# Optimization experiments

Measured on AMD Instinct MI355X. Metric: run time of the kernel, lower is better.

The kernel has to match this reference:

```python
import jax, jax.numpy as jnp
import numpy as np

N_LAYERS = 3
LEAKY_ALPHA = 0.2
NEG_INF = -9e15

U, I, E_ENT, R = 50000, 25000, 80000, 20
D, K, N_EDGES, BATCH = 64, 16, 4000000, 16384


def setup_inputs() -> dict:
    key = jax.random.key(0)
    ks = jax.random.split(key, 16)
    return {
        "users": jax.random.randint(ks[0], (BATCH,), 0, U),
        "items": jax.random.randint(ks[1], (BATCH,), 0, I),
        "g_rows": jax.random.randint(ks[2], (N_EDGES,), 0, U + I, dtype=jnp.int32),
        "g_cols": jax.random.randint(ks[3], (N_EDGES,), 0, U + I, dtype=jnp.int32),
        "g_vals": jax.random.uniform(ks[4], (N_EDGES,), jnp.float32) * (1.0 / 27.0),
        "user_emb": jax.random.normal(ks[5], (U, D), jnp.float32) * 0.1,
        "item_emb": jax.random.normal(ks[6], (I, D), jnp.float32) * 0.1,
        "entity_emb": jax.random.normal(ks[7], (E_ENT + 1, D), jnp.float32) * 0.1,
        "relation_emb": jax.random.normal(ks[8], (R + 1, D), jnp.float32) * 0.1,
        "kg_entities": jax.random.randint(ks[9], (I, K), 0, E_ENT + 1, dtype=jnp.int32),
        "kg_relations": jax.random.randint(ks[10], (I, K), 0, R, dtype=jnp.int32),
        "fc_W": jax.random.normal(ks[11], (2 * D, D), jnp.float32) * (1.0 / np.sqrt(2 * D)),
        "fc_b": jnp.zeros((D,), jnp.float32),
    }


def _gat_item_embs(item_emb, entity_emb, relation_emb, kg_entities, kg_relations, fc_W, fc_b):
    # GAT.forward_relation over fixed-width padded KG neighbor sets
    ent = entity_emb[kg_entities]        # [I, K, D]
    rel = relation_emb[kg_relations]     # [I, K, D]
    Wh = jnp.broadcast_to(item_emb[:, None, :], ent.shape)
    a_input = jnp.concatenate([Wh, ent], axis=-1)           # [I, K, 2D]
    e = jnp.sum((a_input @ fc_W + fc_b) * rel, axis=-1)     # [I, K]
    e = jax.nn.leaky_relu(e, LEAKY_ALPHA)
    mask = kg_entities != (entity_emb.shape[0] - 1)         # padding id == num_entities
    e = jnp.where(mask, e, NEG_INF)
    att = jax.nn.softmax(e, axis=1)                         # softmax per item over neighbors
    return jnp.einsum('ik,ikd->id', att, ent) + item_emb    # residual


def _lightgcn(user_emb, items_kg, g_rows, g_cols, g_vals):
    all_emb = jnp.concatenate([user_emb, items_kg], axis=0)  # [N, D]
    n = all_emb.shape[0]
    acc = all_emb
    for _ in range(N_LAYERS):
        all_emb = jax.ops.segment_sum(g_vals[:, None] * all_emb[g_cols], g_rows, num_segments=n)
        acc = acc + all_emb
    return acc / (N_LAYERS + 1)  # mean over layer outputs


def reference(users, items, g_rows, g_cols, g_vals, user_emb, item_emb,
              entity_emb, relation_emb, kg_entities, kg_relations, fc_W, fc_b):
    items_kg = _gat_item_embs(item_emb, entity_emb, relation_emb,
                              kg_entities, kg_relations, fc_W, fc_b)
    light = _lightgcn(user_emb, items_kg, g_rows, g_cols, g_vals)
    num_users = user_emb.shape[0]
    u = light[users]
    it = light[num_users + items]
    return jnp.sum(u * it, axis=1)  # gamma [batch]
```

## Files before the change

kernel.cpp:

```cpp
#include <hip/hip_runtime.h>

#define D 64
#define NEG_INF -9e15f
#define MAXK 16
#define BSH 6
#define BROWS 64
#define MAXNB 2048
#define SCAP 4096
#define SBSH 4
#define MAXNSB 128
#define SBB 8

__device__ __forceinline__ unsigned short f2bf(float f) {
    unsigned u = __float_as_uint(f);
    return (unsigned short)((u + 0x7FFFu + ((u >> 16) & 1u)) >> 16);
}
__device__ __forceinline__ float bf2f(unsigned short h) {
    return __uint_as_float(((unsigned)h) << 16);
}

__global__ void relpre_kernel(const float* __restrict__ fc_W, const float* __restrict__ fc_b,
                              const float* __restrict__ rel_emb,
                              float* __restrict__ w1r, float* __restrict__ w2r,
                              float* __restrict__ br) {
    int r = blockIdx.x;
    int j = threadIdx.x;
    const float* rr = rel_emb + r * D;
    float s1 = 0.f, s2 = 0.f;
    for (int d = 0; d < D; ++d) {
        float rv = rr[d];
        s1 += fc_W[j * D + d] * rv;
        s2 += fc_W[(D + j) * D + d] * rv;
    }
    w1r[r * D + j] = s1;
    w2r[r * D + j] = s2;
    if (j == 0) {
        float sb = 0.f;
        for (int d = 0; d < D; ++d) sb += fc_b[d] * rr[d];
        br[r] = sb;
    }
}

__global__ void gat16_kernel(const float* __restrict__ item_emb, const float* __restrict__ ent_emb,
                             const int* __restrict__ kg_e, const int* __restrict__ kg_r,
                             const float* __restrict__ w1r, const float* __restrict__ w2r,
                             const float* __restrict__ br,
                             float* __restrict__ x_items, unsigned short* __restrict__ xb_items,
                             int I, int pad_id) {
    const int K = 16;
    int wave = (blockIdx.x * blockDim.x + threadIdx.x) >> 6;
    int lane = threadIdx.x & 63;
    if (wave >= I) return;
    int i = wave;
    float itemv = item_emb[i * D + lane];
    float entv[16], pp[16], brv[16];
    int eidx_[16];
    #pragma unroll
    for (int k = 0; k < K; ++k) {
        int eidx = kg_e[i * K + k];
        int r = kg_r[i * K + k];
        eidx_[k] = eidx;
        float ev = ent_emb[(long)eidx * D + lane];
        entv[k] = ev;
        pp[k] = itemv * w1r[r * D + lane] + ev * w2r[r * D + lane];
        brv[k] = br[r];
    }
    float e[16];
    #pragma unroll
    for (int k = 0; k < K; ++k) {
        float p = pp[k];
        #pragma unroll
        for (int off = 32; off > 0; off >>= 1) p += __shfl_xor(p, off, 64);
        p += brv[k];
        p = p > 0.f ? p : 0.2f * p;
        if (eidx_[k] == pad_id) p = NEG_INF;
        e[k] = p;
    }
    float m = e[0];
    #pragma unroll
    for (int k = 1; k < K; ++k) m = fmaxf(m, e[k]);
    float s = 0.f;
    float att[16];
    #pragma unroll
    for (int k = 0; k < K; ++k) { att[k] = expf(e[k] - m); s += att[k]; }
    float inv = 1.f / s;
    float o = itemv;
    #pragma unroll
    for (int k = 0; k < K; ++k) o += att[k] * inv * entv[k];
    x_items[(long)i * D + lane] = o;
    if (xb_items) xb_items[(long)i * D + lane] = f2bf(o);
}

__global__ void gat_kernel(const float* __restrict__ item_emb, const float* __restrict__ ent_emb,
                           const int* __restrict__ kg_e, const int* __restrict__ kg_r,
                           const float* __restrict__ w1r, const float* __restrict__ w2r,
                           const float* __restrict__ br,
                           float* __restrict__ x_items, unsigned short* __restrict__ xb_items,
                           int I, int K, int pad_id) {
    int wave = (blockIdx.x * blockDim.x + threadIdx.x) >> 6;
    int lane = threadIdx.x & 63;
    if (wave >= I) return;
    int i = wave;
    float itemv = item_emb[i * D + lane];
    float entv[MAXK];
    float e[MAXK];
    for (int k = 0; k < K; ++k) {
        int eidx = kg_e[i * K + k];
        int r = kg_r[i * K + k];
        float ev = ent_emb[(long)eidx * D + lane];
        entv[k] = ev;
        float p = itemv * w1r[r * D + lane] + ev * w2r[r * D + lane];
        #pragma unroll
        for (int off = 32; off > 0; off >>= 1) p += __shfl_xor(p, off, 64);
        p += br[r];
        p = p > 0.f ? p : 0.2f * p;
        if (eidx == pad_id) p = NEG_INF;
        e[k] = p;
    }
    float m = e[0];
    for (int k = 1; k < K; ++k) m = fmaxf(m, e[k]);
    float s = 0.f;
    float att[MAXK];
    for (int k = 0; k < K; ++k) { att[k] = expf(e[k] - m); s += att[k]; }
    float inv = 1.f / s;
    float o = itemv;
    for (int k = 0; k < K; ++k) o += att[k] * inv * entv[k];
    x_items[(long)i * D + lane] = o;
    if (xb_items) xb_items[(long)i * D + lane] = f2bf(o);
}

__global__ void initmark_kernel(const float* __restrict__ user_emb, float* __restrict__ x0,
                                unsigned short* __restrict__ xb,
                                const int* __restrict__ users, const int* __restrict__ items,
                                int* __restrict__ flags, int* __restrict__ rowlist,
                                int* __restrict__ nlist, int U, int B, int n4) {
    int i = blockIdx.x * blockDim.x + threadIdx.x;
    if (i < n4) {
        float4 v = ((const float4*)user_emb)[i];
        ((float4*)x0)[i] = v;
        if (xb) {
            ushort4 m;
            m.x = f2bf(v.x); m.y = f2bf(v.y); m.z = f2bf(v.z); m.w = f2bf(v.w);
            ((ushort4*)xb)[i] = m;
        }
    }
    if (i < B) {
        int r1 = users[i];
        if (atomicExch(&flags[r1], 1) == 0) rowlist[atomicAdd(nlist, 1)] = r1;
        int r2 = U + items[i];
        if (atomicExch(&flags[r2], 1) == 0) rowlist[atomicAdd(nlist, 1)] = r2;
    }
}

__global__ void init_kernel(const float* __restrict__ user_emb,
                            float* __restrict__ x, float* __restrict__ acc,
                            int UD, int ND) {
    for (int idx = blockIdx.x * blockDim.x + threadIdx.x; idx < ND;
         idx += gridDim.x * blockDim.x) {
        float v = (idx < UD) ? user_emb[idx] : x[idx];
        x[idx] = v;
        acc[idx] = v;
    }
}

__global__ void mark_kernel(const int* __restrict__ users, const int* __restrict__ items,
                            int* __restrict__ flags, int* __restrict__ rowlist,
                            int* __restrict__ nlist, int U, int B) {
    int i = blockIdx.x * blockDim.x + threadIdx.x;
    if (i >= B) return;
    int r1 = users[i];
    if (atomicExch(&flags[r1], 1) == 0) rowlist[atomicAdd(nlist, 1)] = r1;
    int r2 = U + items[i];
    if (atomicExch(&flags[r2], 1) == 0) rowlist[atomicAdd(nlist, 1)] = r2;
}

__global__ void bhist_kernel(const int* __restrict__ rows, int* __restrict__ bcnt,
                             int n_edges, int NB) {
    __shared__ int h[MAXNB];
    for (int i = threadIdx.x; i < NB; i += blockDim.x) h[i] = 0;
    __syncthreads();
    for (int e = blockIdx.x * blockDim.x + threadIdx.x; e < n_edges;
         e += gridDim.x * blockDim.x)
        atomicAdd(&h[rows[e] >> BSH], 1);
    __syncthreads();
    for (int i = threadIdx.x; i < NB; i += blockDim.x)
        if (h[i]) atomicAdd(&bcnt[i], h[i]);
}

__global__ void bscan_kernel(const int* __restrict__ bcnt, int* __restrict__ bstart,
                             int* __restrict__ bfill, int* __restrict__ sbfill,
                             int NB, int n_edges) {
    __shared__ int bufA[MAXNB];
    __shared__ int bufB[MAXNB];
    int tid = threadIdx.x;
    int v0 = (tid < NB) ? bcnt[tid] : 0;
    int v1 = (tid + 1024 < NB) ? bcnt[tid + 1024] : 0;
    bufA[tid] = v0;
    bufA[tid + 1024] = v1;
    __syncthreads();
    int* src = bufA;
    int* dst = bufB;
    for (int off = 1; off < MAXNB; off <<= 1) {
        int j0 = tid, j1 = tid + 1024;
        dst[j0] = src[j0] + (j0 >= off ? src[j0 - off] : 0);
        dst[j1] = src[j1] + (j1 >= off ? src[j1 - off] : 0);
        __syncthreads();
        int* t = src; src = dst; dst = t;
    }
    if (tid < NB) {
        int ex = src[tid] - v0;
        bstart[tid] = ex;
        bfill[tid] = ex;
        if ((tid & ((1 << SBSH) - 1)) == 0) sbfill[tid >> SBSH] = ex;
    }
    if (tid + 1024 < NB) {
        int ex = src[tid + 1024] - v1;
        bstart[tid + 1024] = ex;
        bfill[tid + 1024] = ex;
        if (((tid + 1024) & ((1 << SBSH) - 1)) == 0) sbfill[(tid + 1024) >> SBSH] = ex;
    }
    if (tid == 0) bstart[NB] = n_edges;
}

__global__ __launch_bounds__(1024) void
part1_kernel(const int* __restrict__ rows, const int* __restrict__ cols,
             const float* __restrict__ vals,
             int* __restrict__ sbfill, long* __restrict__ etmp,
             int n_edges, int NSB) {
    __shared__ int h[MAXNSB];
    int nb_blocks = gridDim.x;
    int c0 = (int)((long)n_edges * blockIdx.x / nb_blocks);
    int c1 = (int)((long)n_edges * (blockIdx.x + 1) / nb_blocks);
    for (int i = threadIdx.x; i < NSB; i += blockDim.x) h[i] = 0;
    __syncthreads();
    for (int e = c0 + threadIdx.x; e < c1; e += blockDim.x)
        atomicAdd(&h[rows[e] >> (BSH + SBSH)], 1);
    __syncthreads();
    for (int i = threadIdx.x; i < NSB; i += blockDim.x)
        if (h[i]) h[i] = atomicAdd(&sbfill[i], h[i]);
    __syncthreads();
    for (int e = c0 + threadIdx.x; e < c1; e += blockDim.x) {
        int r = rows[e];
        int pos = atomicAdd(&h[r >> (BSH + SBSH)], 1);
        etmp[pos] = ((long)(unsigned)__float_as_int(vals[e]) << 32)
                  | (unsigned)(cols[e] | ((r & (BROWS - 1)) << 20)
                               | (((r >> BSH) & ((1 << SBSH) - 1)) << 26));
    }
}

__global__ __launch_bounds__(256) void
part2_kernel(const long* __restrict__ etmp, const int* __restrict__ bstart,
             int* __restrict__ bfill, long* __restrict__ edges2, int NB) {
    __shared__ int h[1 << SBSH];
    int sb = blockIdx.x / SBB;
    int j  = blockIdx.x % SBB;
    int b0 = sb << SBSH;
    int b1 = b0 + (1 << SBSH); if (b1 > NB) b1 = NB;
    int s = bstart[b0];
    int t = bstart[b1];
    int m = t - s;
    int c0 = s + (int)((long)m * j / SBB);
    int c1 = s + (int)((long)m * (j + 1) / SBB);
    if (threadIdx.x < (1 << SBSH)) h[threadIdx.x] = 0;
    __syncthreads();
    for (int e = c0 + threadIdx.x; e < c1; e += blockDim.x)
        atomicAdd(&h[((int)etmp[e] >> 26) & ((1 << SBSH) - 1)], 1);
    __syncthreads();
    if (threadIdx.x < (1 << SBSH)) {
        int c = h[threadIdx.x];
        if (c) h[threadIdx.x] = atomicAdd(&bfill[b0 + threadIdx.x], c);
    }
    __syncthreads();
    for (int e = c0 + threadIdx.x; e < c1; e += blockDim.x) {
        long v = etmp[e];
        int pos = atomicAdd(&h[((int)v >> 26) & ((1 << SBSH) - 1)], 1);
        edges2[pos] = v;
    }
}

__global__ __launch_bounds__(256) void
part_legacy_kernel(const int* __restrict__ rows, const int* __restrict__ cols,
                   const float* __restrict__ vals,
                   int* __restrict__ bfill, long* __restrict__ etmp,
                   int n_edges, int NB) {
    __shared__ int h[MAXNB];
    int nb_blocks = gridDim.x;
    int c0 = (int)((long)n_edges * blockIdx.x / nb_blocks);
    int c1 = (int)((long)n_edges * (blockIdx.x + 1) / nb_blocks);
    for (int i = threadIdx.x; i < NB; i += blockDim.x) h[i] = 0;
    __syncthreads();
    for (int e = c0 + threadIdx.x; e < c1; e += blockDim.x)
        atomicAdd(&h[rows[e] >> BSH], 1);
    __syncthreads();
    for (int i = threadIdx.x; i < NB; i += blockDim.x)
        if (h[i]) h[i] = atomicAdd(&bfill[i], h[i]);
    __syncthreads();
    for (int e = c0 + threadIdx.x; e < c1; e += blockDim.x) {
        int r = rows[e];
        int pos = atomicAdd(&h[r >> BSH], 1);
        etmp[pos] = ((long)(unsigned)__float_as_int(vals[e]) << 32)
                  | (unsigned)(cols[e] | ((r & (BROWS - 1)) << 20));
    }
}

__global__ __launch_bounds__(256) void
sort_kernel(const long* __restrict__ ein, const int* __restrict__ bstart,
            long* __restrict__ edges, int* __restrict__ row_start,
            int* __restrict__ cnt, int N) {
    __shared__ long obuf[SCAP];
    __shared__ int h[BROWS];
    __shared__ int fill[BROWS];
    int b = blockIdx.x;
    int s = bstart[b];
    int t = bstart[b + 1];
    int m = t - s;
    int tid = threadIdx.x;
    if (tid < BROWS) h[tid] = 0;
    __syncthreads();
    int row0 = b << BSH;
    if (m <= SCAP) {
        for (int i = tid; i < m; i += 256) {
            long v = ein[s + i];
            obuf[i] = v;
            atomicAdd(&h[((int)v >> 20) & (BROWS - 1)], 1);
        }
        __syncthreads();
        if (tid < BROWS) fill[tid] = h[tid];
        __syncthreads();
        for (int o = 1; o < BROWS; o <<= 1) {
            int v = (tid < BROWS && tid >= o) ? fill[tid - o] : 0;
            __syncthreads();
            if (tid < BROWS) fill[tid] += v;
            __syncthreads();
        }
        if (tid < BROWS) {
            int ex = fill[tid] - h[tid];
            int row = row0 + tid;
            if (row < N) { row_start[row] = s + ex; cnt[row] = h[tid]; }
            fill[tid] = s + ex;
        }
        __syncthreads();
        for (int i = tid; i < m; i += 256) {
            long v = obuf[i];
            int r = ((int)v >> 20) & (BROWS - 1);
            edges[atomicAdd(&fill[r], 1)] = v;
        }
    } else {
        for (int i = tid; i < m; i += 256)
            atomicAdd(&h[((int)ein[s + i] >> 20) & (BROWS - 1)], 1);
        __syncthreads();
        if (tid < BROWS) fill[tid] = h[tid];
        __syncthreads();
        for (int o = 1; o < BROWS; o <<= 1) {
            int v = (tid < BROWS && tid >= o) ? fill[tid - o] : 0;
            __syncthreads();
            if (tid < BROWS) fill[tid] += v;
            __syncthreads();
        }
        if (tid < BROWS) {
            int ex = fill[tid] - h[tid];
            int row = row0 + tid;
            if (row < N) { row_start[row] = s + ex; cnt[row] = h[tid]; }
            fill[tid] = s + ex;
        }
        __syncthreads();
        for (int i = tid; i < m; i += 256) {
            long v = ein[s + i];
            int r = ((int)v >> 20) & (BROWS - 1);
            edges[atomicAdd(&fill[r], 1)] = v;
        }
    }
}

__global__ __launch_bounds__(256) void
spmv_bf_kernel(const long* __restrict__ edges, const int* __restrict__ row_start,
               const int* __restrict__ cnt, const unsigned short* __restrict__ xb,
               float* __restrict__ nxt, unsigned short* __restrict__ xbn, int N) {
    int wid = (int)((long)blockIdx.x * blockDim.x + threadIdx.x) >> 6;
    int row = __builtin_amdgcn_readfirstlane(wid);
    int lane = threadIdx.x & 63;
    if (row >= N) return;
    int s = __builtin_amdgcn_readfirstlane(row_start[row]);
    int n = __builtin_amdgcn_readfirstlane(cnt[row]);
    const long* ep = edges + s;
    float sum = 0.f;
    int e = 0;
    for (; e + 16 <= n; e += 16) {
        long q[16];
        float g[16];
        #pragma unroll
        for (int j = 0; j < 16; ++j) q[j] = ep[e + j];
        #pragma unroll
        for (int j = 0; j < 16; ++j)
            g[j] = bf2f(xb[(long)((int)q[j] & 0xFFFFF) * D + lane]);
        #pragma unroll
        for (int j = 0; j < 16; ++j) sum += __int_as_float((int)(q[j] >> 32)) * g[j];
    }
    for (; e + 4 <= n; e += 4) {
        long q[4];
        float g[4];
        #pragma unroll
        for (int j = 0; j < 4; ++j) q[j] = ep[e + j];
        #pragma unroll
        for (int j = 0; j < 4; ++j)
            g[j] = bf2f(xb[(long)((int)q[j] & 0xFFFFF) * D + lane]);
        #pragma unroll
        for (int j = 0; j < 4; ++j) sum += __int_as_float((int)(q[j] >> 32)) * g[j];
    }
    for (; e < n; ++e) {
        long q = ep[e];
        sum += __int_as_float((int)(q >> 32)) * bf2f(xb[(long)((int)q & 0xFFFFF) * D + lane]);
    }
    long o = (long)row * D + lane;
    __builtin_nontemporal_store(sum, &nxt[o]);
    xbn[o] = f2bf(sum);
}

__global__ __launch_bounds__(256) void
spmv_list_bf_kernel(const long* __restrict__ edges, const int* __restrict__ row_start,
                    const int* __restrict__ cnt, const int* __restrict__ rowlist,
                    const int* __restrict__ nlist, const unsigned short* __restrict__ xb,
                    float* __restrict__ nxt) {
    int wid = (int)((long)blockIdx.x * blockDim.x + threadIdx.x) >> 6;
    int nl = __builtin_amdgcn_readfirstlane(nlist[0]);
    if (wid >= nl) return;
    int row = __builtin_amdgcn_readfirstlane(rowlist[wid]);
    int lane = threadIdx.x & 63;
    int s = __builtin_amdgcn_readfirstlane(row_start[row]);
    int n = __builtin_amdgcn_readfirstlane(cnt[row]);
    const long* ep = edges + s;
    float sum = 0.f;
    int e = 0;
    for (; e + 16 <= n; e += 16) {
        long q[16];
        float g[16];
        #pragma unroll
        for (int j = 0; j < 16; ++j) q[j] = ep[e + j];
        #pragma unroll
        for (int j = 0; j < 16; ++j)
            g[j] = bf2f(xb[(long)((int)q[j] & 0xFFFFF) * D + lane]);
        #pragma unroll
        for (int j = 0; j < 16; ++j) sum += __int_as_float((int)(q[j] >> 32)) * g[j];
    }
    for (; e + 4 <= n; e += 4) {
        long q[4];
        float g[4];
        #pragma unroll
        for (int j = 0; j < 4; ++j) q[j] = ep[e + j];
        #pragma unroll
        for (int j = 0; j < 4; ++j)
            g[j] = bf2f(xb[(long)((int)q[j] & 0xFFFFF) * D + lane]);
        #pragma unroll
        for (int j = 0; j < 4; ++j) sum += __int_as_float((int)(q[j] >> 32)) * g[j];
    }
    for (; e < n; ++e) {
        long q = ep[e];
        sum += __int_as_float((int)(q >> 32)) * bf2f(xb[(long)((int)q & 0xFFFFF) * D + lane]);
    }
    __builtin_nontemporal_store(sum, &nxt[(long)row * D + lane]);
}

__global__ __launch_bounds__(256) void
spmv_kernel(const long* __restrict__ edges, const int* __restrict__ row_start,
            const int* __restrict__ cnt, const float* __restrict__ x,
            float* __restrict__ nxt, float* __restrict__ acc, int N) {
    int wid = (int)((long)blockIdx.x * blockDim.x + threadIdx.x) >> 6;
    int row = __builtin_amdgcn_readfirstlane(wid);
    int lane = threadIdx.x & 63;
    if (row >= N) return;
    int s = __builtin_amdgcn_readfirstlane(row_start[row]);
    int n = __builtin_amdgcn_readfirstlane(cnt[row]);
    const long* ep = edges + s;
    float sum = 0.f;
    int e = 0;
    for (; e + 16 <= n; e += 16) {
        long q[16];
        float g[16];
        #pragma unroll
        for (int j = 0; j < 16; ++j) q[j] = ep[e + j];
        #pragma unroll
        for (int j = 0; j < 16; ++j) g[j] = x[(long)((int)q[j] & 0xFFFFF) * D + lane];
        #pragma unroll
        for (int j = 0; j < 16; ++j) sum += __int_as_float((int)(q[j] >> 32)) * g[j];
    }
    for (; e + 4 <= n; e += 4) {
        long q[4];
        float g[4];
        #pragma unroll
        for (int j = 0; j < 4; ++j) q[j] = ep[e + j];
        #pragma unroll
        for (int j = 0; j < 4; ++j) g[j] = x[(long)((int)q[j] & 0xFFFFF) * D + lane];
        #pragma unroll
        for (int j = 0; j < 4; ++j) sum += __int_as_float((int)(q[j] >> 32)) * g[j];
    }
    for (; e < n; ++e) {
        long q = ep[e];
        sum += __int_as_float((int)(q >> 32)) * x[(long)((int)q & 0xFFFFF) * D + lane];
    }
    long o = (long)row * D + lane;
    if (acc) { nxt[o] = sum; acc[o] += sum; }
    else __builtin_nontemporal_store(sum, &nxt[o]);
}

__global__ __launch_bounds__(256) void
spmv_list_kernel(const long* __restrict__ edges, const int* __restrict__ row_start,
                 const int* __restrict__ cnt, const int* __restrict__ rowlist,
                 const int* __restrict__ nlist, const float* __restrict__ x,
                 float* __restrict__ nxt, float* __restrict__ acc) {
    int wid = (int)((long)blockIdx.x * blockDim.x + threadIdx.x) >> 6;
    int nl = __builtin_amdgcn_readfirstlane(nlist[0]);
    if (wid >= nl) return;
    int row = __builtin_amdgcn_readfirstlane(rowlist[wid]);
    int lane = threadIdx.x & 63;
    int s = __builtin_amdgcn_readfirstlane(row_start[row]);
    int n = __builtin_amdgcn_readfirstlane(cnt[row]);
    const long* ep = edges + s;
    float sum = 0.f;
    int e = 0;
    for (; e + 16 <= n; e += 16) {
        long q[16];
        float g[16];
        #pragma unroll
        for (int j = 0; j < 16; ++j) q[j] = ep[e + j];
        #pragma unroll
        for (int j = 0; j < 16; ++j) g[j] = x[(long)((int)q[j] & 0xFFFFF) * D + lane];
        #pragma unroll
        for (int j = 0; j < 16; ++j) sum += __int_as_float((int)(q[j] >> 32)) * g[j];
    }
    for (; e + 4 <= n; e += 4) {
        long q[4];
        float g[4];
        #pragma unroll
        for (int j = 0; j < 4; ++j) q[j] = ep[e + j];
        #pragma unroll
        for (int j = 0; j < 4; ++j) g[j] = x[(long)((int)q[j] & 0xFFFFF) * D + lane];
        #pragma unroll
        for (int j = 0; j < 4; ++j) sum += __int_as_float((int)(q[j] >> 32)) * g[j];
    }
    for (; e < n; ++e) {
        long q = ep[e];
        sum += __int_as_float((int)(q >> 32)) * x[(long)((int)q & 0xFFFFF) * D + lane];
    }
    long o = (long)row * D + lane;
    if (acc) { nxt[o] = sum; acc[o] += sum; }
    else __builtin_nontemporal_store(sum, &nxt[o]);
}

__global__ void dot_kernel(const float* __restrict__ x0, const float* __restrict__ x1,
                           const float* __restrict__ x2, const float* __restrict__ x3,
                           const float* __restrict__ acc,
                           const int* __restrict__ users, const int* __restrict__ items,
                           float* __restrict__ out, int U, int B) {
    int wave = (blockIdx.x * blockDim.x + threadIdx.x) >> 6;
    int lane = threadIdx.x & 63;
    if (wave >= B) return;
    long ou = (long)users[wave] * D + lane;
    long oi = (long)(U + items[wave]) * D + lane;
    float su, si;
    if (acc) {
        su = acc[ou];
        si = acc[oi];
    } else {
        su = x0[ou] + x1[ou] + x2[ou] + x3[ou];
        si = x0[oi] + x1[oi] + x2[oi] + x3[oi];
    }
    float p = su * si;
    #pragma unroll
    for (int off = 32; off > 0; off >>= 1) p += __shfl_xor(p, off, 64);
    if (lane == 0) out[wave] = p * 0.0625f;
}

extern "C" void kernel_launch(void* const* d_in, const int* in_sizes, int n_in,
                              void* d_out, int out_size, void* d_ws, size_t ws_size,
                              hipStream_t stream) {
    const int*   users    = (const int*)  d_in[0];
    const int*   items    = (const int*)  d_in[1];
    const int*   g_rows   = (const int*)  d_in[2];
    const int*   g_cols   = (const int*)  d_in[3];
    const float* g_vals   = (const float*)d_in[4];
    const float* user_emb = (const float*)d_in[5];
    const float* item_emb = (const float*)d_in[6];
    const float* ent_emb  = (const float*)d_in[7];
    const float* rel_emb  = (const float*)d_in[8];
    const int*   kg_e     = (const int*)  d_in[9];
    const int*   kg_r     = (const int*)  d_in[10];
    const float* fc_W     = (const float*)d_in[11];
    const float* fc_b     = (const float*)d_in[12];
    float* out = (float*)d_out;

    int B       = in_sizes[0];
    int n_edges = in_sizes[2];
    int U       = in_sizes[5] / D;
    int I       = in_sizes[6] / D;
    int NE1     = in_sizes[7] / D;
    int NR      = in_sizes[8] / D;
    int K       = in_sizes[9] / I;
    int N  = U + I;
    int ND = N * D;
    int NB = (N + BROWS - 1) >> BSH;
    int NSB = (NB + (1 << SBSH) - 1) >> SBSH;

    size_t small = (size_t)(2 * NR * D + NR + 3 * (NB + 1) + MAXNSB + 4 * N + 1) * 4 + 8192;
    size_t need_def = 4ul * ND * 4 + (size_t)n_edges * 8 + small;
    size_t need_bf  = need_def + 2ul * ND * 2 + 512;
    int deferred = (need_def <= ws_size);
    int usebf    = (need_bf <= ws_size);

    char* basep = (char*)d_ws;
    size_t woff = 0;
    auto alloc = [&](size_t bytes) -> char* {
        char* p = basep + woff;
        woff = (woff + bytes + 255) & ~(size_t)255;
        return p;
    };

    float *x0, *x1, *x2, *x3, *acc;
    long *etmp, *edges2;
    unsigned short *xb0 = nullptr, *xb1 = nullptr;
    if (deferred) {
        x0 = (float*)alloc((size_t)ND * 4);
        x1 = (float*)alloc((size_t)ND * 4);
        x2 = (float*)alloc((size_t)ND * 4);
        x3 = (float*)alloc((size_t)ND * 4);
        acc = nullptr;
        etmp   = (long*)x0;
        edges2 = (long*)x2;
        if (usebf) {
            xb0 = (unsigned short*)alloc((size_t)ND * 2);
            xb1 = (unsigned short*)alloc((size_t)ND * 2);
        }
    } else {
        x0 = (float*)alloc((size_t)ND * 4);
        x1 = (float*)alloc((size_t)ND * 4);
        x2 = x0; x3 = x1;
        acc = (float*)alloc((size_t)ND * 4);
        etmp   = (long*)x0;
        edges2 = nullptr;
        usebf = 0;
    }
    float* w1r      = (float*)alloc((size_t)NR * D * 4);
    float* w2r      = (float*)alloc((size_t)NR * D * 4);
    float* br       = (float*)alloc((size_t)NR * 4);
    int*   bcnt     = (int*)  alloc((size_t)(NB + 1) * 4);
    int*   bstart   = (int*)  alloc((size_t)(NB + 1) * 4);
    int*   bfill    = (int*)  alloc((size_t)(NB + 1) * 4);
    int*   sbfill   = (int*)  alloc((size_t)MAXNSB * 4);
    int*   row_start= (int*)  alloc((size_t)N * 4);
    int*   cnt      = (int*)  alloc((size_t)N * 4);
    int*   flags    = (int*)  alloc((size_t)(N + 1) * 4);
    int*   rowlist  = (int*)  alloc((size_t)N * 4);
    int*   nlist    = flags + N;
    long*  edges    = (long*) alloc((size_t)n_edges * 8);

    hipMemsetAsync(bcnt, 0, (size_t)(NB + 1) * 4, stream);
    bhist_kernel<<<1024, 256, 0, stream>>>(g_rows, bcnt, n_edges, NB);
    bscan_kernel<<<1, 1024, 0, stream>>>(bcnt, bstart, bfill, sbfill, NB, n_edges);
    if (deferred) {
        part1_kernel<<<512, 1024, 0, stream>>>(g_rows, g_cols, g_vals, sbfill, etmp,
                                               n_edges, NSB);
        part2_kernel<<<NSB * SBB, 256, 0, stream>>>(etmp, bstart, bfill, edges2, NB);
        sort_kernel<<<NB, 256, 0, stream>>>(edges2, bstart, edges, row_start, cnt, N);
    } else {
        part_legacy_kernel<<<512, 256, 0, stream>>>(g_rows, g_cols, g_vals, bfill, etmp,
                                                    n_edges, NB);
        sort_kernel<<<NB, 256, 0, stream>>>(etmp, bstart, edges, row_start, cnt, N);
    }

    hipMemsetAsync(flags, 0, (size_t)(N + 1) * 4, stream);

    relpre_kernel<<<NR, D, 0, stream>>>(fc_W, fc_b, rel_emb, w1r, w2r, br);
    unsigned short* xb_items = usebf ? xb0 + (long)U * D : nullptr;
    if (K == 16) {
        gat16_kernel<<<(I + 3) / 4, 256, 0, stream>>>(item_emb, ent_emb, kg_e, kg_r,
                                                      w1r, w2r, br,
                                                      x0 + (long)U * D, xb_items, I, NE1 - 1);
    } else {
        gat_kernel<<<(I + 3) / 4, 256, 0, stream>>>(item_emb, ent_emb, kg_e, kg_r,
                                                    w1r, w2r, br,
                                                    x0 + (long)U * D, xb_items, I, K, NE1 - 1);
    }

    if (deferred) {
        int n4 = U * D / 4;
        int g = n4 > B ? n4 : B;
        initmark_kernel<<<(g + 255) / 256, 256, 0, stream>>>(user_emb, x0,
                                                             usebf ? xb0 : nullptr,
                                                             users, items,
                                                             flags, rowlist, nlist, U, B, n4);
    } else {
        init_kernel<<<2048, 256, 0, stream>>>(user_emb, x0, acc, U * D, ND);
        mark_kernel<<<(B + 255) / 256, 256, 0, stream>>>(users, items, flags, rowlist,
                                                         nlist, U, B);
    }

    long total = (long)N * 64;
    int blocks = (int)((total + 255) / 256);
    int maxrows = (2 * B < N) ? 2 * B : N;
    int lblocks = (int)(((long)maxrows * 64 + 255) / 256);
    if (usebf) {
        spmv_bf_kernel<<<blocks, 256, 0, stream>>>(edges, row_start, cnt, xb0, x1, xb1, N);
        spmv_bf_kernel<<<blocks, 256, 0, stream>>>(edges, row_start, cnt, xb1, x2, xb0, N);
        spmv_list_bf_kernel<<<lblocks, 256, 0, stream>>>(edges, row_start, cnt, rowlist,
                                                         nlist, xb0, x3);
    } else {
        spmv_kernel<<<blocks, 256, 0, stream>>>(edges, row_start, cnt, x0, x1, acc, N);
        spmv_kernel<<<blocks, 256, 0, stream>>>(edges, row_start, cnt, x1, x2, acc, N);
        spmv_list_kernel<<<lblocks, 256, 0, stream>>>(edges, row_start, cnt, rowlist, nlist,
                                                      x2, x3, acc);
    }

    dot_kernel<<<(B + 3) / 4, 256, 0, stream>>>(x0, x1, x2, x3, acc, users, items, out, U, B);
}
```

Measured before the change: 338.8 us.

## Stage partition tiles in shared memory for coalesced super-bucket scatter

Rewrites the first partition pass so that each block processes tiles of 4096 edges. It ranks each edge within its super-bucket using shared atomics and sorts the tile locally in LDS. It then writes runs of consecutive entries to the global temp buffer, replacing the scattered per-edge 8-byte writes. This adds a serial prefix scan by one thread, a binary search per output element, more barriers, 32KB of LDS per block and more global atomics, since there is one per tile rather than one per block.

```diff
diff --git a/kernel.cpp b/kernel.cpp
--- a/kernel.cpp
+++ b/kernel.cpp
@@ -10,6 +10,9 @@
 #define SBSH 4
 #define MAXNSB 128
 #define SBB 8
+#define P1TPB 256
+#define P1EPT 16
+#define P1TILE (P1TPB * P1EPT)
 
 __device__ __forceinline__ unsigned short f2bf(float f) {
     unsigned u = __float_as_uint(f);
@@ -222,29 +225,62 @@
     if (tid == 0) bstart[NB] = n_edges;
 }
 
-__global__ __launch_bounds__(1024) void
+__global__ __launch_bounds__(P1TPB) void
 part1_kernel(const int* __restrict__ rows, const int* __restrict__ cols,
              const float* __restrict__ vals,
              int* __restrict__ sbfill, long* __restrict__ etmp,
              int n_edges, int NSB) {
-    __shared__ int h[MAXNSB];
-    int nb_blocks = gridDim.x;
-    int c0 = (int)((long)n_edges * blockIdx.x / nb_blocks);
-    int c1 = (int)((long)n_edges * (blockIdx.x + 1) / nb_blocks);
-    for (int i = threadIdx.x; i < NSB; i += blockDim.x) h[i] = 0;
-    __syncthreads();
-    for (int e = c0 + threadIdx.x; e < c1; e += blockDim.x)
-        atomicAdd(&h[rows[e] >> (BSH + SBSH)], 1);
-    __syncthreads();
-    for (int i = threadIdx.x; i < NSB; i += blockDim.x)
-        if (h[i]) h[i] = atomicAdd(&sbfill[i], h[i]);
-    __syncthreads();
-    for (int e = c0 + threadIdx.x; e < c1; e += blockDim.x) {
-        int r = rows[e];
-        int pos = atomicAdd(&h[r >> (BSH + SBSH)], 1);
-        etmp[pos] = ((long)(unsigned)__float_as_int(vals[e]) << 32)
-                  | (unsigned)(cols[e] | ((r & (BROWS - 1)) << 20)
-                               | (((r >> BSH) & ((1 << SBSH) - 1)) << 26));
+    __shared__ long staged[P1TILE];
+    __shared__ int tcnt[MAXNSB];
+    __shared__ int toffs[MAXNSB + 1];
+    __shared__ int gbase[MAXNSB];
+    int nb = gridDim.x;
+    int c0 = (int)((long)n_edges * blockIdx.x / nb);
+    int c1 = (int)((long)n_edges * (blockIdx.x + 1) / nb);
+    int tid = threadIdx.x;
+    for (int t0 = c0; t0 < c1; t0 += P1TILE) {
+        for (int i = tid; i < NSB; i += P1TPB) tcnt[i] = 0;
+        __syncthreads();
+        long pay[P1EPT];
+        int sbv[P1EPT];
+        int rnk[P1EPT];
+        #pragma unroll
+        for (int j = 0; j < P1EPT; ++j) {
+            int e = t0 + tid + j * P1TPB;
+            sbv[j] = -1;
+            if (e < c1) {
+                int r = rows[e];
+                int sb = r >> (BSH + SBSH);
+                sbv[j] = sb;
+                pay[j] = ((long)(unsigned)__float_as_int(vals[e]) << 32)
+                       | (unsigned)(cols[e] | ((r & (BROWS - 1)) << 20)
+                                    | (((r >> BSH) & ((1 << SBSH) - 1)) << 26));
+                rnk[j] = atomicAdd(&tcnt[sb], 1);
+            }
+        }
+        __syncthreads();
+        if (tid == 0) {
+            int run = 0;
+            for (int i = 0; i < NSB; ++i) { toffs[i] = run; run += tcnt[i]; }
+            toffs[NSB] = run;
+        }
+        __syncthreads();
+        for (int i = tid; i < NSB; i += P1TPB)
+            if (tcnt[i]) gbase[i] = atomicAdd(&sbfill[i], tcnt[i]);
+        #pragma unroll
+        for (int j = 0; j < P1EPT; ++j)
+            if (sbv[j] >= 0) staged[toffs[sbv[j]] + rnk[j]] = pay[j];
+        __syncthreads();
+        int total = toffs[NSB];
+        for (int i = tid; i < total; i += P1TPB) {
+            int lo = 0, hi = NSB;
+            while (hi - lo > 1) {
+                int mid = (lo + hi) >> 1;
+                if (toffs[mid] <= i) lo = mid; else hi = mid;
+            }
+            etmp[gbase[lo] + (i - toffs[lo])] = staged[i];
+        }
+        __syncthreads();
     }
 }
 
@@ -656,8 +692,8 @@
     bhist_kernel<<<1024, 256, 0, stream>>>(g_rows, bcnt, n_edges, NB);
     bscan_kernel<<<1, 1024, 0, stream>>>(bcnt, bstart, bfill, sbfill, NB, n_edges);
     if (deferred) {
-        part1_kernel<<<512, 1024, 0, stream>>>(g_rows, g_cols, g_vals, sbfill, etmp,
-                                               n_edges, NSB);
+        part1_kernel<<<1024, P1TPB, 0, stream>>>(g_rows, g_cols, g_vals, sbfill, etmp,
+                                                 n_edges, NSB);
         part2_kernel<<<NSB * SBB, 256, 0, stream>>>(etmp, bstart, bfill, edges2, NB);
         sort_kernel<<<NB, 256, 0, stream>>>(edges2, bstart, edges, row_start, cnt, N);
     } else {
```

After: 346.3 us. +2.2%, slower.
